# Performance work log

Measured on AMD Instinct MI355X. Metric: run time of the kernel, lower is better.

## Reference

```python
import jax, jax.numpy as jnp
import numpy as np


def setup_inputs() -> dict:
    key = jax.random.key(0)
    ks = jax.random.split(key, 6)
    B, d, S = 256, 512, 196  # batch, hidden dim, spatial locations (14x14)
    return {
        "memory_state": jax.random.normal(ks[0], (B, d), dtype=jnp.float32),
        "ctrl_state": jax.random.normal(ks[1], (B, d), dtype=jnp.float32),
        "kb_proj": jax.random.normal(ks[2], (B, d, S), dtype=jnp.float32),
        "W_concat": jax.random.normal(ks[3], (d, d), dtype=jnp.float32) * (1.0 / np.sqrt(d)),
        "b_concat": jax.random.normal(ks[4], (d,), dtype=jnp.float32) * 0.01,
        "w_attn": jax.random.normal(ks[5], (d,), dtype=jnp.float32) * (1.0 / np.sqrt(d)),
    }


def reference(memory_state, ctrl_state, kb_proj, W_concat, b_concat, w_attn):
    # I_elements: [B, S, d] -- elementwise gating of knowledge base by memory
    I_t = memory_state[:, :, None] * kb_proj           # [B, d, S]
    I_t = jnp.transpose(I_t, (0, 2, 1))                # [B, S, d]
    # concat_layer (torch Linear: x @ W^T + b) + residual with kb_proj
    concat = jnp.einsum('bsd,ed->bse', I_t, W_concat) + b_concat
    concat = concat + jnp.transpose(kb_proj, (0, 2, 1))  # [B, S, d]
    # attention logits: (concat * ctrl) @ w_attn -> [B, S]
    rai = jnp.einsum('bsd,d->bs', concat * ctrl_state[:, None, :], w_attn)
    rvi = jax.nn.softmax(rai, axis=1)                  # [B, S]
    # attention-weighted sum over spatial locations -> [B, d]
    read_vector = jnp.einsum('bs,bds->bd', rvi, kb_proj)
    return read_vector
```

## Files before the change

kernel.cpp:

```cpp
#include <hip/hip_runtime.h>
#include <math.h>

#define B 256
#define D 512
#define S 196
#define SQ 49
#define NCH 8

__global__ __launch_bounds__(256) void k_gemm(const float* __restrict__ ctrl,
                                              const float* __restrict__ w_attn,
                                              const float* __restrict__ W,
                                              float* __restrict__ gpart) {
    __shared__ float u_s[64][8];
    const int ce = blockIdx.x >> 5;
    const int b0 = (blockIdx.x & 31) * 8;
    const int t = threadIdx.x;
#pragma unroll
    for (int k = t; k < 512; k += 256) {
        const int j = k & 7, el = k >> 3;
        const int e = ce * 64 + el;
        u_s[el][j] = ctrl[(b0 + j) * D + e] * w_attn[e];
    }
    __syncthreads();
    float a0[8], a1[8];
#pragma unroll
    for (int j = 0; j < 8; ++j) { a0[j] = 0.f; a1[j] = 0.f; }
    for (int e0 = 0; e0 < 64; e0 += 4) {
        float w0[4], w1[4];
#pragma unroll
        for (int i = 0; i < 4; ++i) {
            const int e = ce * 64 + e0 + i;
            w0[i] = W[e * D + t];
            w1[i] = W[e * D + t + 256];
        }
#pragma unroll
        for (int i = 0; i < 4; ++i) {
            const float4 ua = *(const float4*)&u_s[e0 + i][0];
            const float4 ub = *(const float4*)&u_s[e0 + i][4];
            a0[0] += ua.x * w0[i]; a0[1] += ua.y * w0[i];
            a0[2] += ua.z * w0[i]; a0[3] += ua.w * w0[i];
            a0[4] += ub.x * w0[i]; a0[5] += ub.y * w0[i];
            a0[6] += ub.z * w0[i]; a0[7] += ub.w * w0[i];
            a1[0] += ua.x * w1[i]; a1[1] += ua.y * w1[i];
            a1[2] += ua.z * w1[i]; a1[3] += ua.w * w1[i];
            a1[4] += ub.x * w1[i]; a1[5] += ub.y * w1[i];
            a1[6] += ub.z * w1[i]; a1[7] += ub.w * w1[i];
        }
    }
#pragma unroll
    for (int j = 0; j < 8; ++j) {
        gpart[((size_t)(b0 + j) * NCH + ce) * D + t]       = a0[j];
        gpart[((size_t)(b0 + j) * NCH + ce) * D + t + 256] = a1[j];
    }
}

__global__ __launch_bounds__(256, 8) void k_logits(const float* __restrict__ kb,
                                                   const float* __restrict__ gpart,
                                                   const float* __restrict__ mem,
                                                   const float* __restrict__ ctrl,
                                                   const float* __restrict__ w_attn,
                                                   float* __restrict__ rai_part) {
    __shared__ float p_s[64];
    __shared__ float part[4][S];
    const int bid = blockIdx.x;
    const int b = bid >> 3, c = bid & 7;
    const int t = threadIdx.x;
    const int w = t >> 6, l = t & 63;
    if (t < 64) {
        const int d = c * 64 + t;
        float s = 0.f;
#pragma unroll
        for (int ce = 0; ce < NCH; ++ce)
            s += gpart[((size_t)b * NCH + ce) * D + d];
        p_s[t] = mem[b * D + d] * s + ctrl[b * D + d] * w_attn[d];
    }
    __syncthreads();
    const float* base = kb + (size_t)b * D * S + (size_t)c * 64 * S;
    if (l < SQ) {
        float4 acc0 = {0,0,0,0}, acc1 = {0,0,0,0}, acc2 = {0,0,0,0}, acc3 = {0,0,0,0};
#pragma unroll 1
        for (int i = 0; i < 4; ++i) {
            const int r = w * 16 + i;
            const float4 v0 = *(const float4*)(base + (size_t)(r     ) * S + 4 * l);
            const float4 v1 = *(const float4*)(base + (size_t)(r +  4) * S + 4 * l);
            const float4 v2 = *(const float4*)(base + (size_t)(r +  8) * S + 4 * l);
            const float4 v3 = *(const float4*)(base + (size_t)(r + 12) * S + 4 * l);
            const float p0 = p_s[r], p1 = p_s[r + 4], p2 = p_s[r + 8], p3 = p_s[r + 12];
            acc0.x += p0 * v0.x; acc0.y += p0 * v0.y; acc0.z += p0 * v0.z; acc0.w += p0 * v0.w;
            acc1.x += p1 * v1.x; acc1.y += p1 * v1.y; acc1.z += p1 * v1.z; acc1.w += p1 * v1.w;
            acc2.x += p2 * v2.x; acc2.y += p2 * v2.y; acc2.z += p2 * v2.z; acc2.w += p2 * v2.w;
            acc3.x += p3 * v3.x; acc3.y += p3 * v3.y; acc3.z += p3 * v3.z; acc3.w += p3 * v3.w;
        }
        part[w][4 * l + 0] = (acc0.x + acc1.x) + (acc2.x + acc3.x);
        part[w][4 * l + 1] = (acc0.y + acc1.y) + (acc2.y + acc3.y);
        part[w][4 * l + 2] = (acc0.z + acc1.z) + (acc2.z + acc3.z);
        part[w][4 * l + 3] = (acc0.w + acc1.w) + (acc2.w + acc3.w);
    }
    __syncthreads();
    if (t < S)
        rai_part[(size_t)bid * S + t] = (part[0][t] + part[1][t]) + (part[2][t] + part[3][t]);
}

__global__ __launch_bounds__(256, 8) void k_wsum(const float* __restrict__ kb,
                                                 const float* __restrict__ rai_part,
                                                 float* __restrict__ out) {
    __shared__ float rvi_s[S];
    __shared__ float redm[4], reds[4];
    const int bid = blockIdx.x;
    const int b = bid >> 3, c = bid & 7;
    const int t = threadIdx.x;
    const int w = t >> 6, l = t & 63;
    float rai = -INFINITY;
    if (t < S) {
        float v = 0.f;
#pragma unroll
        for (int k = 0; k < NCH; ++k)
            v += rai_part[((size_t)b * NCH + k) * S + t];
        rai = v;
    }
    float m = rai;
#pragma unroll
    for (int o = 1; o < 64; o <<= 1) m = fmaxf(m, __shfl_xor(m, o, 64));
    if (l == 0) redm[w] = m;
    __syncthreads();
    m = fmaxf(fmaxf(redm[0], redm[1]), fmaxf(redm[2], redm[3]));
    float ex = (t < S) ? __expf(rai - m) : 0.f;
    float sm = ex;
#pragma unroll
    for (int o = 1; o < 64; o <<= 1) sm += __shfl_xor(sm, o, 64);
    if (l == 0) reds[w] = sm;
    __syncthreads();
    const float li = (reds[0] + reds[1]) + (reds[2] + reds[3]);
    if (t < S) rvi_s[t] = ex / li;
    __syncthreads();

    float4 rv = {0.f, 0.f, 0.f, 0.f};
    if (l < SQ) rv = *(const float4*)&rvi_s[4 * l];
    const float* base = kb + (size_t)b * D * S + (size_t)c * 64 * S;
#pragma unroll 1
    for (int i = 0; i < 4; ++i) {
        const int r = w * 16 + i;
        float a0 = 0.f, a1 = 0.f, a2 = 0.f, a3 = 0.f;
        if (l < SQ) {
            const float4 v0 = *(const float4*)(base + (size_t)(r     ) * S + 4 * l);
            const float4 v1 = *(const float4*)(base + (size_t)(r +  4) * S + 4 * l);
            const float4 v2 = *(const float4*)(base + (size_t)(r +  8) * S + 4 * l);
            const float4 v3 = *(const float4*)(base + (size_t)(r + 12) * S + 4 * l);
            a0 = rv.x * v0.x + rv.y * v0.y + rv.z * v0.z + rv.w * v0.w;
            a1 = rv.x * v1.x + rv.y * v1.y + rv.z * v1.z + rv.w * v1.w;
            a2 = rv.x * v2.x + rv.y * v2.y + rv.z * v2.z + rv.w * v2.w;
            a3 = rv.x * v3.x + rv.y * v3.y + rv.z * v3.z + rv.w * v3.w;
        }
#pragma unroll
        for (int o = 1; o < 64; o <<= 1) {
            a0 += __shfl_xor(a0, o, 64);
            a1 += __shfl_xor(a1, o, 64);
            a2 += __shfl_xor(a2, o, 64);
            a3 += __shfl_xor(a3, o, 64);
        }
        if (l == 0) {
            float* ob = out + (size_t)b * D + c * 64;
            ob[r] = a0; ob[r + 4] = a1; ob[r + 8] = a2; ob[r + 12] = a3;
        }
    }
}

extern "C" void kernel_launch(void* const* d_in, const int* in_sizes, int n_in,
                              void* d_out, int out_size, void* d_ws, size_t ws_size,
                              hipStream_t stream) {
    const float* mem  = (const float*)d_in[0];
    const float* ctrl = (const float*)d_in[1];
    const float* kb   = (const float*)d_in[2];
    const float* W    = (const float*)d_in[3];
    const float* wat  = (const float*)d_in[5];
    float* out = (float*)d_out;

    float* gpart    = (float*)d_ws;
    float* rai_part = gpart + (size_t)B * NCH * D;

    k_gemm  <<<256,     256, 0, stream>>>(ctrl, wat, W, gpart);
    k_logits<<<B * NCH, 256, 0, stream>>>(kb, gpart, mem, ctrl, wat, rai_part);
    k_wsum  <<<B * NCH, 256, 0, stream>>>(kb, rai_part, out);
}
```

Before: 189.6 us.

## Fuse softmax and weighted sum into logits kernel via last-block atomic counter

Merges the logits and weighted-sum kernels into one. A per-batch atomic counter, reset inside the GEMM kernel, picks the last of the 8 chunk blocks to finish, and that block alone runs the softmax and the full 512-row weighted sum for its batch. This removes a kernel launch and lets the second pass over kb_proj hit cache just after the logits pass. In exchange, the final pass for each batch runs serially in one block instead of across 8, which risks a long tail. The logits loop is also restructured into a single fully unrolled accumulator.

```diff
diff --git a/kernel.cpp b/kernel.cpp
--- a/kernel.cpp
+++ b/kernel.cpp
@@ -10,11 +10,13 @@
 __global__ __launch_bounds__(256) void k_gemm(const float* __restrict__ ctrl,
                                               const float* __restrict__ w_attn,
                                               const float* __restrict__ W,
-                                              float* __restrict__ gpart) {
+                                              float* __restrict__ gpart,
+                                              int* __restrict__ cnt) {
     __shared__ float u_s[64][8];
     const int ce = blockIdx.x >> 5;
     const int b0 = (blockIdx.x & 31) * 8;
     const int t = threadIdx.x;
+    if (blockIdx.x == 0) cnt[t] = 0;
 #pragma unroll
     for (int k = t; k < 512; k += 256) {
         const int j = k & 7, el = k >> 3;
@@ -54,18 +56,24 @@
     }
 }
 
-__global__ __launch_bounds__(256, 8) void k_logits(const float* __restrict__ kb,
-                                                   const float* __restrict__ gpart,
-                                                   const float* __restrict__ mem,
-                                                   const float* __restrict__ ctrl,
-                                                   const float* __restrict__ w_attn,
-                                                   float* __restrict__ rai_part) {
+__global__ __launch_bounds__(256) void k_logits_fin(const float* __restrict__ kb,
+                                                    const float* __restrict__ gpart,
+                                                    const float* __restrict__ mem,
+                                                    const float* __restrict__ ctrl,
+                                                    const float* __restrict__ w_attn,
+                                                    float* __restrict__ rai_part,
+                                                    int* __restrict__ cnt,
+                                                    float* __restrict__ out) {
     __shared__ float p_s[64];
     __shared__ float part[4][S];
+    __shared__ float rvi_s[S];
+    __shared__ float redm[4], reds[4];
+    __shared__ int is_last;
     const int bid = blockIdx.x;
     const int b = bid >> 3, c = bid & 7;
     const int t = threadIdx.x;
     const int w = t >> 6, l = t & 63;
+
     if (t < 64) {
         const int d = c * 64 + t;
         float s = 0.f;
@@ -75,41 +83,31 @@
         p_s[t] = mem[b * D + d] * s + ctrl[b * D + d] * w_attn[d];
     }
     __syncthreads();
+
     const float* base = kb + (size_t)b * D * S + (size_t)c * 64 * S;
     if (l < SQ) {
-        float4 acc0 = {0,0,0,0}, acc1 = {0,0,0,0}, acc2 = {0,0,0,0}, acc3 = {0,0,0,0};
-#pragma unroll 1
-        for (int i = 0; i < 4; ++i) {
+        float4 acc = {0.f, 0.f, 0.f, 0.f};
+#pragma unroll
+        for (int i = 0; i < 16; ++i) {
             const int r = w * 16 + i;
-            const float4 v0 = *(const float4*)(base + (size_t)(r     ) * S + 4 * l);
-            const float4 v1 = *(const float4*)(base + (size_t)(r +  4) * S + 4 * l);
-            const float4 v2 = *(const float4*)(base + (size_t)(r +  8) * S + 4 * l);
-            const float4 v3 = *(const float4*)(base + (size_t)(r + 12) * S + 4 * l);
-            const float p0 = p_s[r], p1 = p_s[r + 4], p2 = p_s[r + 8], p3 = p_s[r + 12];
-            acc0.x += p0 * v0.x; acc0.y += p0 * v0.y; acc0.z += p0 * v0.z; acc0.w += p0 * v0.w;
-            acc1.x += p1 * v1.x; acc1.y += p1 * v1.y; acc1.z += p1 * v1.z; acc1.w += p1 * v1.w;
-            acc2.x += p2 * v2.x; acc2.y += p2 * v2.y; acc2.z += p2 * v2.z; acc2.w += p2 * v2.w;
-            acc3.x += p3 * v3.x; acc3.y += p3 * v3.y; acc3.z += p3 * v3.z; acc3.w += p3 * v3.w;
+            const float4 v = *(const float4*)(base + (size_t)r * S + 4 * l);
+            const float pv = p_s[r];
+            acc.x += pv * v.x; acc.y += pv * v.y;
+            acc.z += pv * v.z; acc.w += pv * v.w;
         }
-        part[w][4 * l + 0] = (acc0.x + acc1.x) + (acc2.x + acc3.x);
-        part[w][4 * l + 1] = (acc0.y + acc1.y) + (acc2.y + acc3.y);
-        part[w][4 * l + 2] = (acc0.z + acc1.z) + (acc2.z + acc3.z);
-        part[w][4 * l + 3] = (acc0.w + acc1.w) + (acc2.w + acc3.w);
+        *(float4*)&part[w][4 * l] = acc;
     }
     __syncthreads();
     if (t < S)
-        rai_part[(size_t)bid * S + t] = (part[0][t] + part[1][t]) + (part[2][t] + part[3][t]);
-}
+        rai_part[(size_t)bid * S + t] =
+            (part[0][t] + part[1][t]) + (part[2][t] + part[3][t]);
 
-__global__ __launch_bounds__(256, 8) void k_wsum(const float* __restrict__ kb,
-                                                 const float* __restrict__ rai_part,
-                                                 float* __restrict__ out) {
-    __shared__ float rvi_s[S];
-    __shared__ float redm[4], reds[4];
-    const int bid = blockIdx.x;
-    const int b = bid >> 3, c = bid & 7;
-    const int t = threadIdx.x;
-    const int w = t >> 6, l = t & 63;
+    __threadfence();
+    if (t == 0) is_last = (atomicAdd(&cnt[b], 1) == NCH - 1);
+    __syncthreads();
+    if (!is_last) return;
+    __threadfence();
+
     float rai = -INFINITY;
     if (t < S) {
         float v = 0.f;
@@ -136,16 +134,16 @@
 
     float4 rv = {0.f, 0.f, 0.f, 0.f};
     if (l < SQ) rv = *(const float4*)&rvi_s[4 * l];
-    const float* base = kb + (size_t)b * D * S + (size_t)c * 64 * S;
+    const float* kbb = kb + (size_t)b * D * S;
 #pragma unroll 1
-    for (int i = 0; i < 4; ++i) {
-        const int r = w * 16 + i;
+    for (int i = 0; i < 32; ++i) {
+        const int r = w * 128 + i * 4;
         float a0 = 0.f, a1 = 0.f, a2 = 0.f, a3 = 0.f;
         if (l < SQ) {
-            const float4 v0 = *(const float4*)(base + (size_t)(r     ) * S + 4 * l);
-            const float4 v1 = *(const float4*)(base + (size_t)(r +  4) * S + 4 * l);
-            const float4 v2 = *(const float4*)(base + (size_t)(r +  8) * S + 4 * l);
-            const float4 v3 = *(const float4*)(base + (size_t)(r + 12) * S + 4 * l);
+            const float4 v0 = *(const float4*)(kbb + (size_t)(r    ) * S + 4 * l);
+            const float4 v1 = *(const float4*)(kbb + (size_t)(r + 1) * S + 4 * l);
+            const float4 v2 = *(const float4*)(kbb + (size_t)(r + 2) * S + 4 * l);
+            const float4 v3 = *(const float4*)(kbb + (size_t)(r + 3) * S + 4 * l);
             a0 = rv.x * v0.x + rv.y * v0.y + rv.z * v0.z + rv.w * v0.w;
             a1 = rv.x * v1.x + rv.y * v1.y + rv.z * v1.z + rv.w * v1.w;
             a2 = rv.x * v2.x + rv.y * v2.y + rv.z * v2.z + rv.w * v2.w;
@@ -159,8 +157,8 @@
             a3 += __shfl_xor(a3, o, 64);
         }
         if (l == 0) {
-            float* ob = out + (size_t)b * D + c * 64;
-            ob[r] = a0; ob[r + 4] = a1; ob[r + 8] = a2; ob[r + 12] = a3;
+            float* ob = out + (size_t)b * D + r;
+            ob[0] = a0; ob[1] = a1; ob[2] = a2; ob[3] = a3;
         }
     }
 }
@@ -177,8 +175,9 @@
 
     float* gpart    = (float*)d_ws;
     float* rai_part = gpart + (size_t)B * NCH * D;
+    int*   cnt      = (int*)(rai_part + (size_t)B * NCH * S);
 
-    k_gemm  <<<256,     256, 0, stream>>>(ctrl, wat, W, gpart);
-    k_logits<<<B * NCH, 256, 0, stream>>>(kb, gpart, mem, ctrl, wat, rai_part);
-    k_wsum  <<<B * NCH, 256, 0, stream>>>(kb, rai_part, out);
+    k_gemm      <<<256,     256, 0, stream>>>(ctrl, wat, W, gpart, cnt);
+    k_logits_fin<<<B * NCH, 256, 0, stream>>>(kb, gpart, mem, ctrl, wat,
+                                              rai_part, cnt, out);
 }
```

New measurement: 647.6 us. 241% more time.
